# Kernel tuning notes

Hardware: AMD Instinct MI355X
Metric: run time of the kernel (lower is better)

## Reference

```python
import jax, jax.numpy as jnp
import numpy as np

D_MODEL = 1024
N_HEADS = 16
D_HEAD = D_MODEL // N_HEADS
D_FF = 2048
B, S = 4, 1024
EPS = 1e-6


def layernorm(x, gamma, beta):
    mu = jnp.mean(x, axis=-1, keepdims=True)
    var = jnp.mean(jnp.square(x - mu), axis=-1, keepdims=True)
    return (x - mu) * jax.lax.rsqrt(var + EPS) * gamma + beta


def setup_inputs() -> dict:
    key = jax.random.key(0)
    ks = jax.random.split(key, 12)
    s = 0.02
    return {
        "x": jax.random.normal(ks[0], (B, S, D_MODEL), jnp.float32),
        "mask": jnp.ones((B, 1, 1, S), jnp.int32),
        "Wq": jax.random.normal(ks[1], (D_MODEL, D_MODEL), jnp.float32) * s,
        "Wk": jax.random.normal(ks[2], (D_MODEL, D_MODEL), jnp.float32) * s,
        "Wv": jax.random.normal(ks[3], (D_MODEL, D_MODEL), jnp.float32) * s,
        "Wo": jax.random.normal(ks[4], (D_MODEL, D_MODEL), jnp.float32) * s,
        "bo": jnp.zeros((D_MODEL,), jnp.float32),
        "ln1_g": jnp.ones((D_MODEL,), jnp.float32),
        "ln1_b": jnp.zeros((D_MODEL,), jnp.float32),
        "W1": jax.random.normal(ks[5], (D_MODEL, D_FF), jnp.float32) * s,
        "b1": jnp.zeros((D_FF,), jnp.float32),
        "W2": jax.random.normal(ks[6], (D_FF, D_MODEL), jnp.float32) * s,
        "b2": jnp.zeros((D_MODEL,), jnp.float32),
        "ln2_g": jnp.ones((D_MODEL,), jnp.float32),
        "ln2_b": jnp.zeros((D_MODEL,), jnp.float32),
    }


def reference(x, mask, Wq, Wk, Wv, Wo, bo, ln1_g, ln1_b, W1, b1, W2, b2, ln2_g, ln2_b):
    b, s, _ = x.shape
    # --- multi-head attention ---
    q_proj = x @ Wq                      # [B,S,D]
    k_proj = x @ Wk
    v_proj = x @ Wv
    q = q_proj.reshape(b, s, N_HEADS, D_HEAD)
    k = k_proj.reshape(b, s, N_HEADS, D_HEAD)
    v = v_proj.reshape(b, s, N_HEADS, D_HEAD)
    attn = jnp.einsum('bqhd,bkhd->bhqk', q, k)           # [B,H,S,S]
    attn = jnp.where(mask == 0, -jnp.inf, attn)
    attn = jax.nn.softmax(attn / jnp.sqrt(jnp.float32(D_MODEL)), axis=-1)
    out = jnp.einsum('bhqk,bkhd->bqhd', attn, v).reshape(b, s, D_MODEL)
    # source applies ReLU after the output projection, dropout=eval identity
    out = jax.nn.relu(out @ Wo + bo) + q_proj            # residual = projected queries
    out = layernorm(out, ln1_g, ln1_b)
    # --- FFN (source applies activation AFTER linear2) ---
    ff = jax.nn.relu((out @ W1 + b1) @ W2 + b2) + out
    return layernorm(ff, ln2_g, ln2_b)
```

## Files before the change

### kernel.cpp

```cpp
#include <hip/hip_runtime.h>
#include <hip/hip_bf16.h>

#define D_MODEL 1024
#define N_HEADS 16
#define D_HEAD  64
#define D_FF    2048
#define BATCH   4
#define SEQ     1024
#define ROWS    (BATCH*SEQ)

typedef __bf16  bf16x8 __attribute__((ext_vector_type(8)));
typedef float   f32x4  __attribute__((ext_vector_type(4)));
typedef unsigned int u32x4 __attribute__((ext_vector_type(4)));
typedef unsigned int u32x2 __attribute__((ext_vector_type(2)));
typedef unsigned short u16;
typedef unsigned int u32;

__device__ inline u16 f2bf(float x){ __hip_bfloat16 b = __float2bfloat16(x); return *(u16*)&b; }

__device__ inline void load_lds16(const u16* gsrc, u16* ldst){
  __builtin_amdgcn_global_load_lds((const __attribute__((address_space(1))) void*)gsrc,
                                   (__attribute__((address_space(3))) void*)ldst, 16, 0, 0);
}

__global__ __launch_bounds__(256)
void cast_bf16_kernel(const float* __restrict__ src, __hip_bfloat16* __restrict__ dst, int n){
  int i = (blockIdx.x*blockDim.x + threadIdx.x)*4;
  if (i + 3 < n){
    float4 v = *(const float4*)(src + i);
    dst[i+0] = __float2bfloat16(v.x);
    dst[i+1] = __float2bfloat16(v.y);
    dst[i+2] = __float2bfloat16(v.z);
    dst[i+3] = __float2bfloat16(v.w);
  }
}

__global__ __launch_bounds__(256)
void transpose_cast_kernel(const float* __restrict__ src, __hip_bfloat16* __restrict__ dst,
                           int R, int C){
  __shared__ float tile[32][33];
  int c0 = blockIdx.x*32, r0 = blockIdx.y*32;
  int tx = threadIdx.x & 31, ty = threadIdx.x >> 5;
  #pragma unroll
  for (int i=0;i<32;i+=8)
    tile[ty+i][tx] = src[(size_t)(r0+ty+i)*C + (c0+tx)];
  __syncthreads();
  #pragma unroll
  for (int i=0;i<32;i+=8)
    dst[(size_t)(c0+ty+i)*R + (r0+tx)] = __float2bfloat16(tile[tx][ty+i]);
}

template<int MODE>
__global__ __launch_bounds__(256, 2)
void gemm_bt_kernel(const u16* __restrict__ A, const u16* __restrict__ BT,
                    const float* __restrict__ bias, float* __restrict__ Cf,
                    __hip_bfloat16* __restrict__ Cb, int M, int N, int K, float cscale){
  __shared__ u16 As[128*32];
  __shared__ u16 Bs[128*32];
  const int m0 = blockIdx.y*128, n0 = blockIdx.x*128;
  const int t = threadIdx.x;
  const int wid = t>>6, lane = t&63;
  const int wm = wid>>1, wn = wid&1;
  const int lr = lane&15, lk = (lane>>4)*8;
  const int srow = t>>2, sseg = (t&3)*8;
  const int wbase = wid*512;

  f32x4 acc[4][4] = {};

  for (int kt=0; kt<K; kt+=32){
    __syncthreads();
    #pragma unroll
    for (int c=0;c<2;++c){
      load_lds16(A  + (size_t)(m0 + c*64 + srow)*K + kt + sseg, &As[c*2048 + wbase]);
      load_lds16(BT + (size_t)(n0 + c*64 + srow)*K + kt + sseg, &Bs[c*2048 + wbase]);
    }
    __syncthreads();
    bf16x8 af[4], bfr[4];
    #pragma unroll
    for (int f=0; f<4; ++f){
      af[f]  = *(const bf16x8*)&As[(wm*64 + f*16 + lr)*32 + lk];
      bfr[f] = *(const bf16x8*)&Bs[(wn*64 + f*16 + lr)*32 + lk];
    }
    #pragma unroll
    for (int i=0;i<4;++i)
      #pragma unroll
      for (int j=0;j<4;++j)
        acc[i][j] = __builtin_amdgcn_mfma_f32_16x16x32_bf16(af[i], bfr[j], acc[i][j], 0,0,0);
  }

  const int r_in = (lane>>4)*4;
  #pragma unroll
  for (int i=0;i<4;++i){
    #pragma unroll
    for (int j=0;j<4;++j){
      int col = n0 + wn*64 + j*16 + lr;
      float bv = bias ? bias[col] : 0.f;
      #pragma unroll
      for (int e=0;e<4;++e){
        int row = m0 + wm*64 + i*16 + r_in + e;
        float v = acc[i][j][e] + bv;
        if (MODE == 0){
          Cf[(size_t)row*N + col] = v;
        } else if (MODE == 1){
          Cb[(size_t)row*N + col] = __float2bfloat16(v);
        } else {
          int b = row>>10, s = row&1023;
          int which = col>>10, c = col&1023, h = c>>6, d = c&63;
          size_t hm = (((size_t)b*16 + h)*1024 + s)*64 + d;
          if (which == 0){
            Cf[(size_t)row*1024 + c] = v;
            Cb[hm] = __float2bfloat16(v * cscale);
          } else if (which == 1){
            Cb[4194304u + hm] = __float2bfloat16(v);
          } else {
            Cb[8388608u + (((size_t)b*16 + h)*64 + d)*1024 + s] = __float2bfloat16(v);
          }
        }
      }
    }
  }
}

__global__ __launch_bounds__(512)
void attn_mfma_kernel(const u16* __restrict__ qb, const u16* __restrict__ kb,
                      const u16* __restrict__ vt, const int* __restrict__ mask,
                      __hip_bfloat16* __restrict__ out){
  __shared__ u16 Ks[64*72];
  __shared__ u16 Vs[64*72];
  __shared__ u16 Pl[8][16*72];
  const int t = threadIdx.x;
  const int wid = t>>6, lane = t&63;
  const int lr = lane&15, lg = lane>>4, lk = lg*8;
  const int bh = blockIdx.y;
  const int b = bh>>4, h = bh&15;
  const int q0 = blockIdx.x*128 + wid*16;
  const u16* qbase = qb + (size_t)bh*1024*64;
  const u16* kbase = kb + (size_t)bh*1024*64;
  const u16* vbase = vt + (size_t)bh*64*1024;
  const int* mrow = mask + b*SEQ;

  bf16x8 aq[2];
  aq[0] = *(const bf16x8*)(qbase + (size_t)(q0+lr)*64 + lk);
  aq[1] = *(const bf16x8*)(qbase + (size_t)(q0+lr)*64 + 32 + lk);

  f32x4 osum[4] = {};
  float m1 = -1e30f, l1 = 0.f;

  for (int kt=0; kt<SEQ/64; ++kt){
    const int k0 = kt*64;
    __syncthreads();
    {
      int r = t>>3, sg = (t&7)*8;
      *(u32x4*)&Ks[r*72+sg] = *(const u32x4*)(kbase + (size_t)(k0+r)*64 + sg);
      *(u32x4*)&Vs[r*72+sg] = *(const u32x4*)(vbase + (size_t)r*1024 + k0 + sg);
    }
    __syncthreads();

    unsigned long long bm = __ballot(mrow[k0 + lane] != 0);

    f32x4 sacc[4] = {};
    __builtin_amdgcn_s_setprio(1);
    #pragma unroll
    for (int k4=0;k4<4;++k4){
      #pragma unroll
      for (int dg=0;dg<2;++dg){
        bf16x8 kf = *(const bf16x8*)&Ks[(k4*16+lr)*72 + dg*32 + lk];
        sacc[k4] = __builtin_amdgcn_mfma_f32_16x16x32_bf16(kf, aq[dg], sacc[k4],0,0,0);
      }
    }
    __builtin_amdgcn_s_setprio(0);
    #pragma unroll
    for (int k4=0;k4<4;++k4)
      #pragma unroll
      for (int e=0;e<4;++e)
        if (!((bm >> (k4*16 + lg*4 + e)) & 1)) sacc[k4][e] = -1e30f;

    float tm = -1e30f;
    #pragma unroll
    for (int k4=0;k4<4;++k4)
      #pragma unroll
      for (int e=0;e<4;++e) tm = fmaxf(tm, sacc[k4][e]);
    tm = fmaxf(tm, __shfl_xor(tm,16));
    tm = fmaxf(tm, __shfl_xor(tm,32));
    float mn = fmaxf(m1, tm);
    float c  = __expf(m1 - mn);
    m1 = mn;
    float ps = 0.f;
    #pragma unroll
    for (int k4=0;k4<4;++k4)
      #pragma unroll
      for (int e=0;e<4;++e){ float p = __expf(sacc[k4][e]-mn); sacc[k4][e]=p; ps+=p; }
    ps += __shfl_xor(ps,16);
    ps += __shfl_xor(ps,32);
    l1 = l1*c + ps;

    float ce[4];
    #pragma unroll
    for (int e=0;e<4;++e) ce[e] = __shfl(c, lg*4+e);
    #pragma unroll
    for (int dt=0;dt<4;++dt)
      #pragma unroll
      for (int e=0;e<4;++e) osum[dt][e] *= ce[e];

    #pragma unroll
    for (int k4=0;k4<4;++k4){
      u32 lo = (u32)f2bf(sacc[k4][0]) | ((u32)f2bf(sacc[k4][1])<<16);
      u32 hi = (u32)f2bf(sacc[k4][2]) | ((u32)f2bf(sacc[k4][3])<<16);
      u32x2 pk; pk[0]=lo; pk[1]=hi;
      *(u32x2*)&Pl[wid][lr*72 + k4*16 + lg*4] = pk;
    }
    __builtin_amdgcn_s_setprio(1);
    #pragma unroll
    for (int dt=0;dt<4;++dt){
      #pragma unroll
      for (int kg=0;kg<2;++kg){
        bf16x8 pa = *(const bf16x8*)&Pl[wid][lr*72 + kg*32 + lk];
        bf16x8 vf = *(const bf16x8*)&Vs[(dt*16+lr)*72 + kg*32 + lk];
        osum[dt] = __builtin_amdgcn_mfma_f32_16x16x32_bf16(pa, vf, osum[dt],0,0,0);
      }
    }
    __builtin_amdgcn_s_setprio(0);
  }
  float li[4];
  #pragma unroll
  for (int e=0;e<4;++e) li[e] = 1.f / __shfl(l1, lg*4+e);
  #pragma unroll
  for (int dt=0;dt<4;++dt){
    int d = dt*16 + lr;
    #pragma unroll
    for (int e=0;e<4;++e){
      int q = q0 + lg*4 + e;
      out[((size_t)b*1024 + q)*1024 + h*64 + d] = __float2bfloat16(osum[dt][e] * li[e]);
    }
  }
}

__global__ __launch_bounds__(256)
void ln_fused_kernel(const float* __restrict__ a, const float* __restrict__ res,
                     const float* __restrict__ g, const float* __restrict__ be,
                     float* __restrict__ outf, __hip_bfloat16* __restrict__ outb){
  int row = blockIdx.x, t = threadIdx.x;
  size_t rb = (size_t)row*D_MODEL;
  float4 av = *(const float4*)(a  + rb + t*4);
  float4 rv = *(const float4*)(res+ rb + t*4);
  float v0 = fmaxf(av.x,0.f)+rv.x;
  float v1 = fmaxf(av.y,0.f)+rv.y;
  float v2 = fmaxf(av.z,0.f)+rv.z;
  float v3 = fmaxf(av.w,0.f)+rv.w;
  float sum = v0+v1+v2+v3;
  float ss  = v0*v0+v1*v1+v2*v2+v3*v3;
  #pragma unroll
  for (int off=32; off; off>>=1){ sum += __shfl_xor(sum,off); ss += __shfl_xor(ss,off); }
  __shared__ float red[8];
  int wid = t>>6, lane = t&63;
  if (lane==0){ red[wid]=sum; red[4+wid]=ss; }
  __syncthreads();
  sum = red[0]+red[1]+red[2]+red[3];
  ss  = red[4]+red[5]+red[6]+red[7];
  float mu  = sum*(1.f/1024.f);
  float var = ss*(1.f/1024.f) - mu*mu;
  float rstd = rsqrtf(var + 1e-6f);
  float4 gv = *(const float4*)(g  + t*4);
  float4 bv = *(const float4*)(be + t*4);
  float y0=(v0-mu)*rstd*gv.x+bv.x;
  float y1=(v1-mu)*rstd*gv.y+bv.y;
  float y2=(v2-mu)*rstd*gv.z+bv.z;
  float y3=(v3-mu)*rstd*gv.w+bv.w;
  *(float4*)(outf+rb+t*4) = make_float4(y0,y1,y2,y3);
  if (outb){
    outb[rb+t*4+0]=__float2bfloat16(y0);
    outb[rb+t*4+1]=__float2bfloat16(y1);
    outb[rb+t*4+2]=__float2bfloat16(y2);
    outb[rb+t*4+3]=__float2bfloat16(y3);
  }
}

extern "C" void kernel_launch(void* const* d_in, const int* in_sizes, int n_in,
                              void* d_out, int out_size, void* d_ws, size_t ws_size,
                              hipStream_t stream){
  const float* x    = (const float*)d_in[0];
  const int*   mask = (const int*)  d_in[1];
  const float* Wq   = (const float*)d_in[2];
  const float* Wk   = (const float*)d_in[3];
  const float* Wv   = (const float*)d_in[4];
  const float* Wo   = (const float*)d_in[5];
  const float* bo   = (const float*)d_in[6];
  const float* ln1g = (const float*)d_in[7];
  const float* ln1b = (const float*)d_in[8];
  const float* W1   = (const float*)d_in[9];
  const float* b1   = (const float*)d_in[10];
  const float* W2   = (const float*)d_in[11];
  const float* b2   = (const float*)d_in[12];
  const float* ln2g = (const float*)d_in[13];
  const float* ln2b = (const float*)d_in[14];

  char* ws = (char*)d_ws;
  const size_t MB = 1024*1024;
  __hip_bfloat16* WqT  = (__hip_bfloat16*)(ws + 0);
  __hip_bfloat16* WkT  = (__hip_bfloat16*)(ws + 2*MB);
  __hip_bfloat16* WvT  = (__hip_bfloat16*)(ws + 4*MB);
  __hip_bfloat16* WoT  = (__hip_bfloat16*)(ws + 6*MB);
  __hip_bfloat16* W1T  = (__hip_bfloat16*)(ws + 8*MB);
  __hip_bfloat16* W2T  = (__hip_bfloat16*)(ws + 12*MB);
  __hip_bfloat16* xb   = (__hip_bfloat16*)(ws + 16*MB);
  float* q_proj        = (float*)(ws + 24*MB);
  __hip_bfloat16* qb   = (__hip_bfloat16*)(ws + 40*MB);
  __hip_bfloat16* attn_o = (__hip_bfloat16*)(ws + 64*MB);
  float* proj_o        = (float*)(ws + 40*MB);
  float* h1f           = (float*)(ws + 56*MB);
  __hip_bfloat16* h1b  = (__hip_bfloat16*)(ws + 16*MB);
  __hip_bfloat16* ff1b = (__hip_bfloat16*)(ws + 24*MB);
  float* ff2           = (float*)(ws + 40*MB);

  const float qscale = 0.03125f;

  cast_bf16_kernel<<<ROWS*D_MODEL/4/256, 256, 0, stream>>>(x, xb, ROWS*D_MODEL);
  transpose_cast_kernel<<<dim3(32,32), 256, 0, stream>>>(Wq, WqT, 1024, 1024);
  transpose_cast_kernel<<<dim3(32,32), 256, 0, stream>>>(Wk, WkT, 1024, 1024);
  transpose_cast_kernel<<<dim3(32,32), 256, 0, stream>>>(Wv, WvT, 1024, 1024);
  transpose_cast_kernel<<<dim3(32,32), 256, 0, stream>>>(Wo, WoT, 1024, 1024);
  transpose_cast_kernel<<<dim3(64,32), 256, 0, stream>>>(W1, W1T, 1024, 2048);
  transpose_cast_kernel<<<dim3(32,64), 256, 0, stream>>>(W2, W2T, 2048, 1024);

  gemm_bt_kernel<5><<<dim3(24,32), 256, 0, stream>>>((const u16*)xb, (const u16*)WqT, nullptr,
                                                     q_proj, qb, ROWS, 3072, 1024, qscale);

  attn_mfma_kernel<<<dim3(SEQ/128, BATCH*N_HEADS), 512, 0, stream>>>(
      (const u16*)qb, (const u16*)(qb + 4194304u), (const u16*)(qb + 8388608u), mask, attn_o);

  gemm_bt_kernel<0><<<dim3(8,32), 256, 0, stream>>>((const u16*)attn_o, (const u16*)WoT, bo,
                                                    proj_o, nullptr, ROWS, 1024, 1024, 1.f);

  ln_fused_kernel<<<ROWS, 256, 0, stream>>>(proj_o, q_proj, ln1g, ln1b, h1f, h1b);

  gemm_bt_kernel<1><<<dim3(16,32), 256, 0, stream>>>((const u16*)h1b, (const u16*)W1T, b1,
                                                     nullptr, ff1b, ROWS, 2048, 1024, 1.f);

  gemm_bt_kernel<0><<<dim3(8,32), 256, 0, stream>>>((const u16*)ff1b, (const u16*)W2T, b2,
                                                    ff2, nullptr, ROWS, 1024, 2048, 1.f);

  ln_fused_kernel<<<ROWS, 256, 0, stream>>>(ff2, h1f, ln2g, ln2b, (float*)d_out, nullptr);
}
```

Measured before the change: 228.0 us.

## Batch weight transposes, deepen GEMM K step, lazy softmax rescale with exp2

Merges the four 1024x1024 weight transpose-casts into a single launch with a z-dimension. The GEMM now loads two 32-wide K slices per barrier pair, so there are half as many syncs, at the cost of twice the shared memory. Attention folds log2(e) into the query scale so it can use exp2f. It also skips the mask pass when the whole mask word is set. The running-max rescale of the accumulator is skipped unless the new max exceeds the old one by more than 8 in log2 units, which trades some numerical headroom for fewer exp and multiply operations.

Result: faster. 215.7 us (-5.4%).

```diff
diff --git a/kernel.cpp b/kernel.cpp
--- a/kernel.cpp
+++ b/kernel.cpp
@@ -50,13 +50,31 @@
     dst[(size_t)(c0+ty+i)*R + (r0+tx)] = __float2bfloat16(tile[tx][ty+i]);
 }
 
+__global__ __launch_bounds__(256)
+void transpose4_kernel(const float* __restrict__ s0, const float* __restrict__ s1,
+                       const float* __restrict__ s2, const float* __restrict__ s3,
+                       __hip_bfloat16* __restrict__ dst){
+  __shared__ float tile[32][33];
+  const float* src = (blockIdx.z==0)?s0:(blockIdx.z==1)?s1:(blockIdx.z==2)?s2:s3;
+  __hip_bfloat16* d = dst + (size_t)blockIdx.z*1024*1024;
+  int c0 = blockIdx.x*32, r0 = blockIdx.y*32;
+  int tx = threadIdx.x & 31, ty = threadIdx.x >> 5;
+  #pragma unroll
+  for (int i=0;i<32;i+=8)
+    tile[ty+i][tx] = src[(size_t)(r0+ty+i)*1024 + (c0+tx)];
+  __syncthreads();
+  #pragma unroll
+  for (int i=0;i<32;i+=8)
+    d[(size_t)(c0+ty+i)*1024 + (r0+tx)] = __float2bfloat16(tile[tx][ty+i]);
+}
+
 template<int MODE>
 __global__ __launch_bounds__(256, 2)
 void gemm_bt_kernel(const u16* __restrict__ A, const u16* __restrict__ BT,
                     const float* __restrict__ bias, float* __restrict__ Cf,
                     __hip_bfloat16* __restrict__ Cb, int M, int N, int K, float cscale){
-  __shared__ u16 As[128*32];
-  __shared__ u16 Bs[128*32];
+  __shared__ u16 As[2][128*32];
+  __shared__ u16 Bs[2][128*32];
   const int m0 = blockIdx.y*128, n0 = blockIdx.x*128;
   const int t = threadIdx.x;
   const int wid = t>>6, lane = t&63;
@@ -67,25 +85,31 @@
 
   f32x4 acc[4][4] = {};
 
-  for (int kt=0; kt<K; kt+=32){
+  for (int kt=0; kt<K; kt+=64){
     __syncthreads();
     #pragma unroll
-    for (int c=0;c<2;++c){
-      load_lds16(A  + (size_t)(m0 + c*64 + srow)*K + kt + sseg, &As[c*2048 + wbase]);
-      load_lds16(BT + (size_t)(n0 + c*64 + srow)*K + kt + sseg, &Bs[c*2048 + wbase]);
+    for (int half=0; half<2; ++half){
+      #pragma unroll
+      for (int c=0;c<2;++c){
+        load_lds16(A  + (size_t)(m0 + c*64 + srow)*K + kt + half*32 + sseg, &As[half][c*2048 + wbase]);
+        load_lds16(BT + (size_t)(n0 + c*64 + srow)*K + kt + half*32 + sseg, &Bs[half][c*2048 + wbase]);
+      }
     }
     __syncthreads();
-    bf16x8 af[4], bfr[4];
-    #pragma unroll
-    for (int f=0; f<4; ++f){
-      af[f]  = *(const bf16x8*)&As[(wm*64 + f*16 + lr)*32 + lk];
-      bfr[f] = *(const bf16x8*)&Bs[(wn*64 + f*16 + lr)*32 + lk];
-    }
-    #pragma unroll
-    for (int i=0;i<4;++i)
-      #pragma unroll
-      for (int j=0;j<4;++j)
-        acc[i][j] = __builtin_amdgcn_mfma_f32_16x16x32_bf16(af[i], bfr[j], acc[i][j], 0,0,0);
+    #pragma unroll
+    for (int half=0; half<2; ++half){
+      bf16x8 af[4], bfr[4];
+      #pragma unroll
+      for (int f=0; f<4; ++f){
+        af[f]  = *(const bf16x8*)&As[half][(wm*64 + f*16 + lr)*32 + lk];
+        bfr[f] = *(const bf16x8*)&Bs[half][(wn*64 + f*16 + lr)*32 + lk];
+      }
+      #pragma unroll
+      for (int i=0;i<4;++i)
+        #pragma unroll
+        for (int j=0;j<4;++j)
+          acc[i][j] = __builtin_amdgcn_mfma_f32_16x16x32_bf16(af[i], bfr[j], acc[i][j], 0,0,0);
+    }
   }
 
   const int r_in = (lane>>4)*4;
@@ -169,11 +193,13 @@
       }
     }
     __builtin_amdgcn_s_setprio(0);
-    #pragma unroll
-    for (int k4=0;k4<4;++k4)
-      #pragma unroll
-      for (int e=0;e<4;++e)
-        if (!((bm >> (k4*16 + lg*4 + e)) & 1)) sacc[k4][e] = -1e30f;
+    if (bm != ~0ull){
+      #pragma unroll
+      for (int k4=0;k4<4;++k4)
+        #pragma unroll
+        for (int e=0;e<4;++e)
+          if (!((bm >> (k4*16 + lg*4 + e)) & 1)) sacc[k4][e] = -1e30f;
+    }
 
     float tm = -1e30f;
     #pragma unroll
@@ -182,25 +208,32 @@
       for (int e=0;e<4;++e) tm = fmaxf(tm, sacc[k4][e]);
     tm = fmaxf(tm, __shfl_xor(tm,16));
     tm = fmaxf(tm, __shfl_xor(tm,32));
-    float mn = fmaxf(m1, tm);
-    float c  = __expf(m1 - mn);
-    m1 = mn;
+
+    float mn = m1, c = 1.f;
+    bool need = !__all(tm <= m1 + 8.f);
+    if (need){
+      mn = fmaxf(m1, tm);
+      c  = exp2f(m1 - mn);
+      m1 = mn;
+    }
     float ps = 0.f;
     #pragma unroll
     for (int k4=0;k4<4;++k4)
       #pragma unroll
-      for (int e=0;e<4;++e){ float p = __expf(sacc[k4][e]-mn); sacc[k4][e]=p; ps+=p; }
+      for (int e=0;e<4;++e){ float p = exp2f(sacc[k4][e]-mn); sacc[k4][e]=p; ps+=p; }
     ps += __shfl_xor(ps,16);
     ps += __shfl_xor(ps,32);
     l1 = l1*c + ps;
 
-    float ce[4];
-    #pragma unroll
-    for (int e=0;e<4;++e) ce[e] = __shfl(c, lg*4+e);
-    #pragma unroll
-    for (int dt=0;dt<4;++dt)
-      #pragma unroll
-      for (int e=0;e<4;++e) osum[dt][e] *= ce[e];
+    if (need){
+      float ce[4];
+      #pragma unroll
+      for (int e=0;e<4;++e) ce[e] = __shfl(c, lg*4+e);
+      #pragma unroll
+      for (int dt=0;dt<4;++dt)
+        #pragma unroll
+        for (int e=0;e<4;++e) osum[dt][e] *= ce[e];
+    }
 
     #pragma unroll
     for (int k4=0;k4<4;++k4){
@@ -297,8 +330,6 @@
   char* ws = (char*)d_ws;
   const size_t MB = 1024*1024;
   __hip_bfloat16* WqT  = (__hip_bfloat16*)(ws + 0);
-  __hip_bfloat16* WkT  = (__hip_bfloat16*)(ws + 2*MB);
-  __hip_bfloat16* WvT  = (__hip_bfloat16*)(ws + 4*MB);
   __hip_bfloat16* WoT  = (__hip_bfloat16*)(ws + 6*MB);
   __hip_bfloat16* W1T  = (__hip_bfloat16*)(ws + 8*MB);
   __hip_bfloat16* W2T  = (__hip_bfloat16*)(ws + 12*MB);
@@ -312,13 +343,10 @@
   __hip_bfloat16* ff1b = (__hip_bfloat16*)(ws + 24*MB);
   float* ff2           = (float*)(ws + 40*MB);
 
-  const float qscale = 0.03125f;
+  const float qscale = 0.03125f * 1.44269504f;
 
   cast_bf16_kernel<<<ROWS*D_MODEL/4/256, 256, 0, stream>>>(x, xb, ROWS*D_MODEL);
-  transpose_cast_kernel<<<dim3(32,32), 256, 0, stream>>>(Wq, WqT, 1024, 1024);
-  transpose_cast_kernel<<<dim3(32,32), 256, 0, stream>>>(Wk, WkT, 1024, 1024);
-  transpose_cast_kernel<<<dim3(32,32), 256, 0, stream>>>(Wv, WvT, 1024, 1024);
-  transpose_cast_kernel<<<dim3(32,32), 256, 0, stream>>>(Wo, WoT, 1024, 1024);
+  transpose4_kernel<<<dim3(32,32,4), 256, 0, stream>>>(Wq, Wk, Wv, Wo, WqT);
   transpose_cast_kernel<<<dim3(64,32), 256, 0, stream>>>(W1, W1T, 1024, 2048);
   transpose_cast_kernel<<<dim3(32,64), 256, 0, stream>>>(W2, W2T, 2048, 1024);
 
```
